# Performance work log

Hardware: AMD Instinct MI355X
Metric: run time of the kernel (lower is better)

Reference implementation:

```python
import jax, jax.numpy as jnp
import numpy as np

EPS = 1e-5
QMAX = 127.0


def setup_inputs() -> dict:
    key = jax.random.key(0)
    k1, k2, k3, k4, k5 = jax.random.split(key, 5)
    B, S, N = 2, 4096, 4096
    x1 = jax.random.normal(k1, (B, S, N), dtype=jnp.float32)
    x2 = jax.random.normal(k2, (B, S, N), dtype=jnp.float32)
    gamma = jax.random.normal(k3, (N,), dtype=jnp.float32)
    # smoothing scales are positive channel-wise multipliers
    smooth_scale1 = jax.random.uniform(k4, (N,), dtype=jnp.float32, minval=0.5, maxval=1.5)
    smooth_scale2 = jax.random.uniform(k5, (N,), dtype=jnp.float32, minval=0.5, maxval=1.5)
    return {"x1": x1, "x2": x2, "gamma": gamma,
            "smooth_scale1": smooth_scale1, "smooth_scale2": smooth_scale2}


def _dynamic_quant(y, smooth_scale):
    # per-row (last-axis) dynamic symmetric int8 quantization after smoothing
    ys = y * smooth_scale                       # [..., N]
    scale = jnp.max(jnp.abs(ys), axis=-1, keepdims=True) / QMAX  # [..., 1]
    yq = jnp.clip(jnp.round(ys / scale), -128.0, 127.0).astype(jnp.int8)
    return yq, scale[..., 0]


def reference(x1, x2, gamma, smooth_scale1, smooth_scale2):
    # fused residual add
    x_sum = x1 + x2                             # [B, S, N]
    # RMSNorm over the last axis with weight gamma
    inv_rms = jax.lax.rsqrt(jnp.mean(x_sum * x_sum, axis=-1, keepdims=True) + EPS)
    y_norm = x_sum * inv_rms * gamma            # [B, S, N]
    # dual smooth-quant with independent dynamic per-row scales
    y1, scale1 = _dynamic_quant(y_norm, smooth_scale1)
    y2, scale2 = _dynamic_quant(y_norm, smooth_scale2)
    return (x_sum, y_norm, y1, scale1, y2, scale2)
```

## Files before the change

### kernel.cpp

```cpp
#include <hip/hip_runtime.h>

#define NCOLS 4096
#define QMAXF 127.0f
#define EPSF 1e-5f

__global__ __launch_bounds__(256) void fused_addrms_dualquant(
    const float* __restrict__ x1,
    const float* __restrict__ x2,
    const float* __restrict__ gamma,
    const float* __restrict__ sm1,
    const float* __restrict__ sm2,
    float* __restrict__ o_xsum,
    float* __restrict__ o_ynorm,
    float* __restrict__ o_y1,
    float* __restrict__ o_s1,
    float* __restrict__ o_y2,
    float* __restrict__ o_s2)
{
    const int row = blockIdx.x;
    const long long base = (long long)row * NCOLS;
    const int t = threadIdx.x;

    float4 s[4];
    float ssq = 0.f;
#pragma unroll
    for (int c = 0; c < 4; ++c) {
        const int idx = c * 1024 + t * 4;
        float4 a = *(const float4*)(x1 + base + idx);
        float4 b = *(const float4*)(x2 + base + idx);
        float4 v;
        v.x = a.x + b.x; v.y = a.y + b.y; v.z = a.z + b.z; v.w = a.w + b.w;
        s[c] = v;
        ssq += v.x * v.x + v.y * v.y + v.z * v.z + v.w * v.w;
        *(float4*)(o_xsum + base + idx) = v;
    }

#pragma unroll
    for (int off = 32; off > 0; off >>= 1) ssq += __shfl_down(ssq, off);

    __shared__ float red[4];
    __shared__ float s_invrms;
    if ((t & 63) == 0) red[t >> 6] = ssq;
    __syncthreads();
    if (t == 0) {
        float tot = red[0] + red[1] + red[2] + red[3];
        s_invrms = rsqrtf(tot * (1.0f / (float)NCOLS) + EPSF);
    }
    __syncthreads();
    const float inv_rms = s_invrms;

    float4 ys1[4], ys2[4];
    float a1 = 0.f, a2 = 0.f;
#pragma unroll
    for (int c = 0; c < 4; ++c) {
        const int idx = c * 1024 + t * 4;
        float4 g  = *(const float4*)(gamma + idx);
        float4 m1 = *(const float4*)(sm1 + idx);
        float4 m2 = *(const float4*)(sm2 + idx);
        float4 y;
        y.x = s[c].x * inv_rms * g.x;
        y.y = s[c].y * inv_rms * g.y;
        y.z = s[c].z * inv_rms * g.z;
        y.w = s[c].w * inv_rms * g.w;
        *(float4*)(o_ynorm + base + idx) = y;
        ys1[c].x = y.x * m1.x; ys1[c].y = y.y * m1.y;
        ys1[c].z = y.z * m1.z; ys1[c].w = y.w * m1.w;
        ys2[c].x = y.x * m2.x; ys2[c].y = y.y * m2.y;
        ys2[c].z = y.z * m2.z; ys2[c].w = y.w * m2.w;
        a1 = fmaxf(a1, fmaxf(fmaxf(fabsf(ys1[c].x), fabsf(ys1[c].y)),
                             fmaxf(fabsf(ys1[c].z), fabsf(ys1[c].w))));
        a2 = fmaxf(a2, fmaxf(fmaxf(fabsf(ys2[c].x), fabsf(ys2[c].y)),
                             fmaxf(fabsf(ys2[c].z), fabsf(ys2[c].w))));
    }

#pragma unroll
    for (int off = 32; off > 0; off >>= 1) {
        a1 = fmaxf(a1, __shfl_down(a1, off));
        a2 = fmaxf(a2, __shfl_down(a2, off));
    }
    __shared__ float redm1[4], redm2[4];
    __shared__ float s_sc1, s_sc2;
    if ((t & 63) == 0) { redm1[t >> 6] = a1; redm2[t >> 6] = a2; }
    __syncthreads();
    if (t == 0) {
        float m1v = fmaxf(fmaxf(redm1[0], redm1[1]), fmaxf(redm1[2], redm1[3]));
        float m2v = fmaxf(fmaxf(redm2[0], redm2[1]), fmaxf(redm2[2], redm2[3]));
        float sc1 = m1v / QMAXF;
        float sc2 = m2v / QMAXF;
        o_s1[row] = sc1;
        o_s2[row] = sc2;
        s_sc1 = sc1;
        s_sc2 = sc2;
    }
    __syncthreads();
    const float sc1 = s_sc1, sc2 = s_sc2;

#pragma unroll
    for (int c = 0; c < 4; ++c) {
        const int idx = c * 1024 + t * 4;
        float4 q1, q2;
        q1.x = fminf(fmaxf(rintf(ys1[c].x / sc1), -128.f), 127.f);
        q1.y = fminf(fmaxf(rintf(ys1[c].y / sc1), -128.f), 127.f);
        q1.z = fminf(fmaxf(rintf(ys1[c].z / sc1), -128.f), 127.f);
        q1.w = fminf(fmaxf(rintf(ys1[c].w / sc1), -128.f), 127.f);
        q2.x = fminf(fmaxf(rintf(ys2[c].x / sc2), -128.f), 127.f);
        q2.y = fminf(fmaxf(rintf(ys2[c].y / sc2), -128.f), 127.f);
        q2.z = fminf(fmaxf(rintf(ys2[c].z / sc2), -128.f), 127.f);
        q2.w = fminf(fmaxf(rintf(ys2[c].w / sc2), -128.f), 127.f);
        *(float4*)(o_y1 + base + idx) = q1;
        *(float4*)(o_y2 + base + idx) = q2;
    }
}

extern "C" void kernel_launch(void* const* d_in, const int* in_sizes, int n_in,
                              void* d_out, int out_size, void* d_ws, size_t ws_size,
                              hipStream_t stream) {
    const float* x1    = (const float*)d_in[0];
    const float* x2    = (const float*)d_in[1];
    const float* gamma = (const float*)d_in[2];
    const float* sm1   = (const float*)d_in[3];
    const float* sm2   = (const float*)d_in[4];

    const long long n_elem = in_sizes[0];
    const int ncols = in_sizes[2];
    const long long rows = n_elem / ncols;

    float* out = (float*)d_out;
    float* o_xsum  = out;
    float* o_ynorm = out + n_elem;
    float* o_y1    = out + 2 * n_elem;
    float* o_s1    = out + 3 * n_elem;
    float* o_y2    = o_s1 + rows;
    float* o_s2    = o_y2 + n_elem;

    fused_addrms_dualquant<<<dim3((unsigned)rows), dim3(256), 0, stream>>>(
        x1, x2, gamma, sm1, sm2, o_xsum, o_ynorm, o_y1, o_s1, o_y2, o_s2);
}
```

Before: 691.9 us.

## Merge RMS and absmax reductions into one pass with nontemporal streaming accesses

The row's absolute maxima are now computed on the unnormalized gamma-scaled values, using the fact that inv_rms is a positive scalar, so the sum-of-squares and both max reductions share one shuffle pass and one barrier pair. The quantization divides become multiplies by precomputed reciprocals, and streaming loads and stores use nontemporal hints. The aim is to cut a synchronization round and the register pressure from keeping ys1/ys2, in exchange for reloading gamma and the smooth scales and for possible last-bit differences in rounding.

```diff
diff --git a/kernel.cpp b/kernel.cpp
--- a/kernel.cpp
+++ b/kernel.cpp
@@ -3,6 +3,8 @@
 #define NCOLS 4096
 #define QMAXF 127.0f
 #define EPSF 1e-5f
+
+typedef float f4 __attribute__((ext_vector_type(4)));
 
 __global__ __launch_bounds__(256) void fused_addrms_dualquant(
     const float* __restrict__ x1,
@@ -21,94 +23,88 @@
     const long long base = (long long)row * NCOLS;
     const int t = threadIdx.x;
 
-    float4 s[4];
-    float ssq = 0.f;
+    f4 v[4];
+    float ssq = 0.f, a1 = 0.f, a2 = 0.f;
+
 #pragma unroll
     for (int c = 0; c < 4; ++c) {
         const int idx = c * 1024 + t * 4;
-        float4 a = *(const float4*)(x1 + base + idx);
-        float4 b = *(const float4*)(x2 + base + idx);
-        float4 v;
-        v.x = a.x + b.x; v.y = a.y + b.y; v.z = a.z + b.z; v.w = a.w + b.w;
-        s[c] = v;
-        ssq += v.x * v.x + v.y * v.y + v.z * v.z + v.w * v.w;
-        *(float4*)(o_xsum + base + idx) = v;
-    }
+        f4 xa = __builtin_nontemporal_load((const f4*)(x1 + base + idx));
+        f4 xb = __builtin_nontemporal_load((const f4*)(x2 + base + idx));
+        f4 s = xa + xb;
+        v[c] = s;
+        ssq += s.x * s.x + s.y * s.y + s.z * s.z + s.w * s.w;
+        __builtin_nontemporal_store(s, (f4*)(o_xsum + base + idx));
 
-#pragma unroll
-    for (int off = 32; off > 0; off >>= 1) ssq += __shfl_down(ssq, off);
-
-    __shared__ float red[4];
-    __shared__ float s_invrms;
-    if ((t & 63) == 0) red[t >> 6] = ssq;
-    __syncthreads();
-    if (t == 0) {
-        float tot = red[0] + red[1] + red[2] + red[3];
-        s_invrms = rsqrtf(tot * (1.0f / (float)NCOLS) + EPSF);
-    }
-    __syncthreads();
-    const float inv_rms = s_invrms;
-
-    float4 ys1[4], ys2[4];
-    float a1 = 0.f, a2 = 0.f;
-#pragma unroll
-    for (int c = 0; c < 4; ++c) {
-        const int idx = c * 1024 + t * 4;
-        float4 g  = *(const float4*)(gamma + idx);
-        float4 m1 = *(const float4*)(sm1 + idx);
-        float4 m2 = *(const float4*)(sm2 + idx);
-        float4 y;
-        y.x = s[c].x * inv_rms * g.x;
-        y.y = s[c].y * inv_rms * g.y;
-        y.z = s[c].z * inv_rms * g.z;
-        y.w = s[c].w * inv_rms * g.w;
-        *(float4*)(o_ynorm + base + idx) = y;
-        ys1[c].x = y.x * m1.x; ys1[c].y = y.y * m1.y;
-        ys1[c].z = y.z * m1.z; ys1[c].w = y.w * m1.w;
-        ys2[c].x = y.x * m2.x; ys2[c].y = y.y * m2.y;
-        ys2[c].z = y.z * m2.z; ys2[c].w = y.w * m2.w;
-        a1 = fmaxf(a1, fmaxf(fmaxf(fabsf(ys1[c].x), fabsf(ys1[c].y)),
-                             fmaxf(fabsf(ys1[c].z), fabsf(ys1[c].w))));
-        a2 = fmaxf(a2, fmaxf(fmaxf(fabsf(ys2[c].x), fabsf(ys2[c].y)),
-                             fmaxf(fabsf(ys2[c].z), fabsf(ys2[c].w))));
+        f4 g  = *(const f4*)(gamma + idx);
+        f4 m1 = *(const f4*)(sm1 + idx);
+        f4 m2 = *(const f4*)(sm2 + idx);
+        f4 gg = s * g;
+        f4 p1 = gg * m1;
+        f4 p2 = gg * m2;
+        a1 = fmaxf(a1, fmaxf(fmaxf(fabsf(p1.x), fabsf(p1.y)),
+                             fmaxf(fabsf(p1.z), fabsf(p1.w))));
+        a2 = fmaxf(a2, fmaxf(fmaxf(fabsf(p2.x), fabsf(p2.y)),
+                             fmaxf(fabsf(p2.z), fabsf(p2.w))));
     }
 
 #pragma unroll
     for (int off = 32; off > 0; off >>= 1) {
+        ssq += __shfl_down(ssq, off);
         a1 = fmaxf(a1, __shfl_down(a1, off));
         a2 = fmaxf(a2, __shfl_down(a2, off));
     }
-    __shared__ float redm1[4], redm2[4];
-    __shared__ float s_sc1, s_sc2;
-    if ((t & 63) == 0) { redm1[t >> 6] = a1; redm2[t >> 6] = a2; }
+
+    __shared__ float red[12];
+    __shared__ float bc[3];
+    if ((t & 63) == 0) {
+        const int w = t >> 6;
+        red[w]     = ssq;
+        red[4 + w] = a1;
+        red[8 + w] = a2;
+    }
     __syncthreads();
     if (t == 0) {
-        float m1v = fmaxf(fmaxf(redm1[0], redm1[1]), fmaxf(redm1[2], redm1[3]));
-        float m2v = fmaxf(fmaxf(redm2[0], redm2[1]), fmaxf(redm2[2], redm2[3]));
-        float sc1 = m1v / QMAXF;
-        float sc2 = m2v / QMAXF;
+        float tot = red[0] + red[1] + red[2] + red[3];
+        float invrms = rsqrtf(tot * (1.0f / (float)NCOLS) + EPSF);
+        float am1 = fmaxf(fmaxf(red[4], red[5]), fmaxf(red[6], red[7])) * invrms;
+        float am2 = fmaxf(fmaxf(red[8], red[9]), fmaxf(red[10], red[11])) * invrms;
+        float sc1 = am1 / QMAXF;
+        float sc2 = am2 / QMAXF;
         o_s1[row] = sc1;
         o_s2[row] = sc2;
-        s_sc1 = sc1;
-        s_sc2 = sc2;
+        bc[0] = invrms;
+        bc[1] = 1.0f / sc1;
+        bc[2] = 1.0f / sc2;
     }
     __syncthreads();
-    const float sc1 = s_sc1, sc2 = s_sc2;
+    const float invrms = bc[0];
+    const float r1 = bc[1];
+    const float r2 = bc[2];
 
 #pragma unroll
     for (int c = 0; c < 4; ++c) {
         const int idx = c * 1024 + t * 4;
-        float4 q1, q2;
-        q1.x = fminf(fmaxf(rintf(ys1[c].x / sc1), -128.f), 127.f);
-        q1.y = fminf(fmaxf(rintf(ys1[c].y / sc1), -128.f), 127.f);
-        q1.z = fminf(fmaxf(rintf(ys1[c].z / sc1), -128.f), 127.f);
-        q1.w = fminf(fmaxf(rintf(ys1[c].w / sc1), -128.f), 127.f);
-        q2.x = fminf(fmaxf(rintf(ys2[c].x / sc2), -128.f), 127.f);
-        q2.y = fminf(fmaxf(rintf(ys2[c].y / sc2), -128.f), 127.f);
-        q2.z = fminf(fmaxf(rintf(ys2[c].z / sc2), -128.f), 127.f);
-        q2.w = fminf(fmaxf(rintf(ys2[c].w / sc2), -128.f), 127.f);
-        *(float4*)(o_y1 + base + idx) = q1;
-        *(float4*)(o_y2 + base + idx) = q2;
+        f4 g  = *(const f4*)(gamma + idx);
+        f4 m1 = *(const f4*)(sm1 + idx);
+        f4 m2 = *(const f4*)(sm2 + idx);
+
+        f4 y = v[c] * invrms * g;
+        __builtin_nontemporal_store(y, (f4*)(o_ynorm + base + idx));
+
+        f4 ys1 = y * m1;
+        f4 ys2 = y * m2;
+        f4 q1, q2;
+        q1.x = fminf(fmaxf(rintf(ys1.x * r1), -128.f), 127.f);
+        q1.y = fminf(fmaxf(rintf(ys1.y * r1), -128.f), 127.f);
+        q1.z = fminf(fmaxf(rintf(ys1.z * r1), -128.f), 127.f);
+        q1.w = fminf(fmaxf(rintf(ys1.w * r1), -128.f), 127.f);
+        q2.x = fminf(fmaxf(rintf(ys2.x * r2), -128.f), 127.f);
+        q2.y = fminf(fmaxf(rintf(ys2.y * r2), -128.f), 127.f);
+        q2.z = fminf(fmaxf(rintf(ys2.z * r2), -128.f), 127.f);
+        q2.w = fminf(fmaxf(rintf(ys2.w * r2), -128.f), 127.f);
+        __builtin_nontemporal_store(q1, (f4*)(o_y1 + base + idx));
+        __builtin_nontemporal_store(q2, (f4*)(o_y2 + base + idx));
     }
 }
 
```

After: 687.1 us. Within noise of the previous version (-0.7%).
